# Kernel optimization log

Hardware: AMD Instinct MI355X
Metric: run time of the kernel (lower is better)

The kernel has to match this reference:

```python
import jax, jax.numpy as jnp
import numpy as np

J = 25
C_IN, HID, LAT = 3, 64, 32


def _graph_conv(x, A, W, b):
    # x: [N,T,J,Cin]; A: [J,J]; W: [Cin,Cout]; b: [Cout]
    A = jax.nn.softmax(A, axis=-1)
    # fused adjacency mix + projection: (A @ x) @ W + b
    x = jnp.einsum('ij,ntjc->ntic', A, x)
    return jnp.einsum('ntjc,cd->ntjd', x, W) + b


def setup_inputs() -> dict:
    key = jax.random.key(0)
    ks = jax.random.split(key, 13)
    x = jax.random.normal(ks[0], (32, 2048, J, C_IN), dtype=jnp.float32)
    eye = jnp.eye(J, dtype=jnp.float32)
    def lin(kw, kb, cin, cout):
        W = jax.random.normal(kw, (cin, cout), dtype=jnp.float32) / np.sqrt(cin)
        b = jax.random.normal(kb, (cout,), dtype=jnp.float32) * 0.01
        return W, b
    W1, b1 = lin(ks[1], ks[2], C_IN, HID)
    W2, b2 = lin(ks[3], ks[4], HID, LAT)
    W3, b3 = lin(ks[5], ks[6], LAT, HID)
    W4, b4 = lin(ks[7], ks[8], HID, C_IN)
    return {
        'x': x,
        'A1': eye, 'W1': W1, 'b1': b1,
        'A2': eye, 'W2': W2, 'b2': b2,
        'A3': eye, 'W3': W3, 'b3': b3,
        'A4': eye, 'W4': W4, 'b4': b4,
    }


def reference(x, A1, W1, b1, A2, W2, b2, A3, W3, b3, A4, W4, b4):
    h = jax.nn.relu(_graph_conv(x, A1, W1, b1))     # encoder_g1 + relu
    z = _graph_conv(h, A2, W2, b2)                  # encoder_g2 (no relu)
    h_dec = jax.nn.relu(_graph_conv(z, A3, W3, b3)) # decoder_g1 + relu
    out = _graph_conv(h_dec, A4, W4, b4)            # decoder_g2
    return out
```

## Files before the change

### kernel.cpp

```cpp
#include <hip/hip_runtime.h>
#include <math.h>

#define J 25
#define NJC 75
#define NWAVE 4
#define NTHREADS 256
#define NFPW 8
#define SCRW 1056

#define O_A1T  0
#define O_APP  1024
#define O_A4B  2048
#define O_W2T  3072
#define O_W3T  5120
#define O_W1T  7168
#define O_W4C  8192
#define O_BPPB 8448
#define O_B4   8512

using bf16x4 = __attribute__((ext_vector_type(4))) __bf16;
using bf16x8 = __attribute__((ext_vector_type(8))) __bf16;
using f32x16 = __attribute__((ext_vector_type(16))) float;

__device__ inline bf16x8 zero8() {
    bf16x8 z;
    #pragma unroll
    for (int j = 0; j < 8; j++) z[j] = (__bf16)0.f;
    return z;
}

__device__ inline unsigned pkbf(float a, float b) {
    union { __bf16 h; unsigned short u; } ua, ub;
    ua.h = (__bf16)a; ub.h = (__bf16)b;
    return (unsigned)ua.u | ((unsigned)ub.u << 16);
}

__device__ inline void cswap(const f32x16 acc, int half, int lx,
                             bf16x8* f0, bf16x8* f1) {
    const unsigned p0 = pkbf(acc[0],  acc[1]),  p1 = pkbf(acc[2],  acc[3]);
    const unsigned p2 = pkbf(acc[4],  acc[5]),  p3 = pkbf(acc[6],  acc[7]);
    const unsigned p4 = pkbf(acc[8],  acc[9]),  p5 = pkbf(acc[10], acc[11]);
    const unsigned p6 = pkbf(acc[12], acc[13]), p7 = pkbf(acc[14], acc[15]);
    const unsigned s0 = half ? p0 : p2, s1 = half ? p1 : p3;
    const unsigned s2 = half ? p4 : p6, s3 = half ? p5 : p7;
    const unsigned r0 = (unsigned)__shfl((int)s0, lx, 64);
    const unsigned r1 = (unsigned)__shfl((int)s1, lx, 64);
    const unsigned r2 = (unsigned)__shfl((int)s2, lx, 64);
    const unsigned r3 = (unsigned)__shfl((int)s3, lx, 64);
    uint4 u0, u1;
    u0.x = half ? r0 : p0;  u0.y = half ? r1 : p1;
    u0.z = half ? p2 : r0;  u0.w = half ? p3 : r1;
    u1.x = half ? r2 : p4;  u1.y = half ? r3 : p5;
    u1.z = half ? p6 : r2;  u1.w = half ? p7 : r3;
    *f0 = *(bf16x8*)&u0;  *f1 = *(bf16x8*)&u1;
}

__global__ void gcn_precompute(
    const float* __restrict__ A1, const float* __restrict__ W1, const float* __restrict__ b1,
    const float* __restrict__ A2, const float* __restrict__ W2, const float* __restrict__ b2,
    const float* __restrict__ A3, const float* __restrict__ W3, const float* __restrict__ b3,
    const float* __restrict__ A4, const float* __restrict__ W4, const float* __restrict__ b4,
    __bf16* __restrict__ cw)
{
    __shared__ float T[3125];
    __shared__ float bpp[64];
    float* T0 = T;        float* T1 = T + 625;  float* T2 = T + 1250;
    float* T3 = T + 1875; float* T4 = T + 2500;
    const int t = threadIdx.x;

    if (t < 100) {
        const int m = t / J, i = t % J;
        const float* Asrc = (m == 0) ? A1 : (m == 1) ? A2 : (m == 2) ? A3 : A4;
        float row[J];
        float mx = -1e30f;
        #pragma unroll
        for (int j = 0; j < J; j++) { row[j] = Asrc[i * J + j]; mx = fmaxf(mx, row[j]); }
        float s = 0.f;
        #pragma unroll
        for (int j = 0; j < J; j++) { row[j] = __expf(row[j] - mx); s += row[j]; }
        const float inv = 1.f / s;
        float* dst = T + m * 625 + i * J;
        #pragma unroll
        for (int j = 0; j < J; j++) dst[j] = row[j] * inv;
    }
    if (t < 64) {
        float s = b3[t];
        #pragma unroll
        for (int l = 0; l < 32; l++) s += W3[l * 64 + t] * b2[l];
        bpp[t] = s;
    }
    __syncthreads();

    for (int idx = t; idx < 625; idx += 256) {
        const int i = idx / J, jj = idx % J;
        float s = 0.f;
        #pragma unroll
        for (int k = 0; k < J; k++) s += T2[i * J + k] * T1[k * J + jj];
        T4[idx] = s;
    }
    __syncthreads();

    for (int i = t; i < 1024; i += 256) {
        const int b = i >> 8, n = (i >> 3) & 31, jj = i & 7, j = 8 * b + jj;
        const bool ok = (j < J) && (n < J);
        cw[O_A1T + i] = (__bf16)(ok ? T0[n * J + j] : 0.f);
        cw[O_APP + i] = (__bf16)(ok ? T4[n * J + j] : 0.f);
        cw[O_A4B + i] = (__bf16)(ok ? T3[n * J + j] : 0.f);
    }
    for (int i = t; i < 2048; i += 256) {
        const int b = i >> 8, m = (i >> 3) & 31, jj = i & 7;
        cw[O_W2T + i] = (__bf16)W2[(8 * b + jj) * 32 + m];
        const int tt = i >> 10, r = i & 1023;
        const int b3i = r >> 8, m3 = (r >> 3) & 31, j3 = r & 7;
        cw[O_W3T + i] = (__bf16)W3[(8 * b3i + j3) * 64 + tt * 32 + m3];
    }
    for (int i = t; i < 1024; i += 256) {
        const int tt = i >> 9, r = i & 511, hf = r >> 8, q = r & 255;
        const int m = q >> 3, c = q & 7, d = tt * 32 + m;
        float v = 0.f;
        if (hf == 0) {
            if (c < 3) v = W1[c * 64 + d];
            else if (c == 3) v = b1[d];
        }
        cw[O_W1T + i] = (__bf16)v;
    }
    if (t < 256)
        cw[O_W4C + t] = (t < 192) ? (__bf16)W4[(t & 63) * 3 + (t >> 6)] : (__bf16)0.f;

    if (t < 64) {
        const int tt = t >> 5, rem = t & 31, hf = rem >> 4, q = rem & 15;
        const int g = q >> 2, r2 = q & 3;
        cw[O_BPPB + t] = (__bf16)bpp[tt * 32 + 8 * g + 4 * hf + r2];
    }
    float* fb4 = (float*)(cw + O_B4);
    if (t >= 64 && t < 68) fb4[t - 64] = (t < 67) ? b4[t - 64] : 0.f;
}

__global__ __launch_bounds__(NTHREADS, 3) void gcn_fused(
    const float* __restrict__ x,
    const __bf16* __restrict__ cw,
    float* __restrict__ out)
{
    __shared__ __align__(16) __bf16 SCR[NWAVE * SCRW];

    const int t = threadIdx.x;
    const int w = t >> 6, lane = t & 63, ln = lane & 31, half = lane >> 5;
    const int lx = lane ^ 32;
    const int fo = ln * 8;
    __bf16* sc = &SCR[w * SCRW];

    const long fbase = ((long)blockIdx.x * NWAVE + w) * NFPW;

    long xb = fbase * NJC;
    float xv0 = x[xb + lane];
    float xv1 = (lane < NJC - 64) ? x[xb + 64 + lane] : 0.f;

    bf16x8 rA1T[2], rApp[2], rA4b[2], rW1[2], rW2[4], rW3[4], rW4[4], rBpp[4];
    #pragma unroll
    for (int ks = 0; ks < 2; ks++) {
        rA1T[ks] = *(const bf16x8*)&cw[O_A1T + (2 * ks + half) * 256 + fo];
        rApp[ks] = *(const bf16x8*)&cw[O_APP + (2 * ks + half) * 256 + fo];
        rA4b[ks] = *(const bf16x8*)&cw[O_A4B + (2 * ks + half) * 256 + fo];
        rW1[ks]  = *(const bf16x8*)&cw[O_W1T + ks * 512 + half * 256 + fo];
    }
    #pragma unroll
    for (int ks = 0; ks < 4; ks++)
        rW2[ks] = *(const bf16x8*)&cw[O_W2T + (half + 2 * ks) * 256 + fo];
    #pragma unroll
    for (int tt = 0; tt < 2; tt++)
        #pragma unroll
        for (int ks = 0; ks < 2; ks++)
            rW3[tt * 2 + ks] = *(const bf16x8*)&cw[O_W3T + tt * 1024 + (half + 2 * ks) * 256 + fo];
    #pragma unroll
    for (int ks = 0; ks < 4; ks++) {
        rW4[ks] = zero8();
        if (ln < 3) rW4[ks] = *(const bf16x8*)&cw[O_W4C + ln * 64 + (half + 2 * ks) * 8];
    }
    #pragma unroll
    for (int tt = 0; tt < 2; tt++)
        #pragma unroll
        for (int p = 0; p < 2; p++)
            rBpp[tt * 2 + p] = *(const bf16x8*)&cw[O_BPPB + (tt * 2 + half) * 16 + p * 8];
    float b4v = 0.f;
    if (ln < 3) b4v = ((const float*)(cw + O_B4))[ln];

    f32x16 Z;
    #pragma unroll
    for (int z = 0; z < 16; z++) Z[z] = 0.f;

    for (int fi = 0; fi < NFPW; fi++) {
        const long f = fbase + fi;

        {
            const int i0 = lane, c0 = i0 % 3, j0 = i0 / 3;
            sc[(j0 >> 3) * 264 + c0 * 8 + (j0 & 7)] = (__bf16)xv0;
            if (lane < NJC - 64) {
                const int i1 = 64 + lane, c1 = i1 % 3, j1 = i1 / 3;
                sc[(j1 >> 3) * 264 + c1 * 8 + (j1 & 7)] = (__bf16)xv1;
            }
            if (half == 0) sc[(ln >> 3) * 264 + 24 + (ln & 7)] = (ln < J) ? (__bf16)1.f : (__bf16)0.f;
            if (lane < 21) sc[3 * 264 + (lane / 7) * 8 + 1 + (lane % 7)] = (__bf16)0.f;
        }

        float nxv0 = 0.f, nxv1 = 0.f;
        if (fi + 1 < NFPW) {
            const long nxb = (f + 1) * NJC;
            nxv0 = x[nxb + lane];
            if (lane < NJC - 64) nxv1 = x[nxb + 64 + lane];
        }

        f32x16 accY;
        {
            bf16x8 a0 = *(const bf16x8*)&sc[half * 264 + fo];
            accY = __builtin_amdgcn_mfma_f32_32x32x16_bf16(a0, rA1T[0], Z, 0, 0, 0);
            bf16x8 a1 = *(const bf16x8*)&sc[(2 + half) * 264 + fo];
            accY = __builtin_amdgcn_mfma_f32_32x32x16_bf16(a1, rA1T[1], accY, 0, 0, 0);
        }

        bf16x8 yb;
        #pragma unroll
        for (int jj = 0; jj < 8; jj++)
            yb[jj] = (half == 0 && jj < 4) ? (__bf16)accY[jj] : (__bf16)0.f;
        bf16x8 hf[4];
        #pragma unroll
        for (int tt = 0; tt < 2; tt++) {
            f32x16 acc = __builtin_amdgcn_mfma_f32_32x32x16_bf16(rW1[tt], yb, Z, 0, 0, 0);
            #pragma unroll
            for (int z = 0; z < 16; z++) acc[z] = fmaxf(acc[z], 0.f);
            cswap(acc, half, lx, &hf[tt * 2], &hf[tt * 2 + 1]);
        }

        f32x16 accU = __builtin_amdgcn_mfma_f32_32x32x16_bf16(hf[0], rW2[0], Z, 0, 0, 0);
        #pragma unroll
        for (int ks = 1; ks < 4; ks++)
            accU = __builtin_amdgcn_mfma_f32_32x32x16_bf16(hf[ks], rW2[ks], accU, 0, 0, 0);
        bf16x8 uf[2];
        cswap(accU, half, lx, &uf[0], &uf[1]);

        f32x16 accV = __builtin_amdgcn_mfma_f32_32x32x16_bf16(uf[0], rApp[0], Z, 0, 0, 0);
        accV = __builtin_amdgcn_mfma_f32_32x32x16_bf16(uf[1], rApp[1], accV, 0, 0, 0);
        bf16x8 vf[2];
        cswap(accV, half, lx, &vf[0], &vf[1]);

        bf16x8 hd[4];
        #pragma unroll
        for (int tt = 0; tt < 2; tt++) {
            f32x16 acc = __builtin_amdgcn_mfma_f32_32x32x16_bf16(rW3[tt * 2 + 0], vf[0], Z, 0, 0, 0);
            acc = __builtin_amdgcn_mfma_f32_32x32x16_bf16(rW3[tt * 2 + 1], vf[1], acc, 0, 0, 0);
            #pragma unroll
            for (int q = 0; q < 16; q++) {
                const float bias = (float)rBpp[tt * 2 + (q >> 3)][q & 7];
                acc[q] = fmaxf(acc[q] + bias, 0.f);
            }
            cswap(acc, half, lx, &hd[tt * 2], &hd[tt * 2 + 1]);
        }

        f32x16 accP = __builtin_amdgcn_mfma_f32_32x32x16_bf16(hd[0], rW4[0], Z, 0, 0, 0);
        #pragma unroll
        for (int ks = 1; ks < 4; ks++)
            accP = __builtin_amdgcn_mfma_f32_32x32x16_bf16(hd[ks], rW4[ks], accP, 0, 0, 0);
        bf16x8 pf[2];
        cswap(accP, half, lx, &pf[0], &pf[1]);

        f32x16 accO = __builtin_amdgcn_mfma_f32_32x32x16_bf16(rA4b[0], pf[0], Z, 0, 0, 0);
        accO = __builtin_amdgcn_mfma_f32_32x32x16_bf16(rA4b[1], pf[1], accO, 0, 0, 0);
        if (ln < 3) {
            const long ob = f * NJC;
            #pragma unroll
            for (int r = 0; r < 16; r++) {
                const int row = (r & 3) + 8 * (r >> 2) + 4 * half;
                if (row < J) out[ob + row * 3 + ln] = accO[r] + b4v;
            }
        }

        xv0 = nxv0; xv1 = nxv1;
    }
}

extern "C" void kernel_launch(void* const* d_in, const int* in_sizes, int n_in,
                              void* d_out, int out_size, void* d_ws, size_t ws_size,
                              hipStream_t stream)
{
    const float* x  = (const float*)d_in[0];
    const float* A1 = (const float*)d_in[1];
    const float* W1 = (const float*)d_in[2];
    const float* b1 = (const float*)d_in[3];
    const float* A2 = (const float*)d_in[4];
    const float* W2 = (const float*)d_in[5];
    const float* b2 = (const float*)d_in[6];
    const float* A3 = (const float*)d_in[7];
    const float* W3 = (const float*)d_in[8];
    const float* b3 = (const float*)d_in[9];
    const float* A4 = (const float*)d_in[10];
    const float* W4 = (const float*)d_in[11];
    const float* b4 = (const float*)d_in[12];
    float* out = (float*)d_out;
    __bf16* cw = (__bf16*)d_ws;

    const int NT = in_sizes[0] / NJC;
    const int nblocks = NT / (NWAVE * NFPW);

    gcn_precompute<<<1, 256, 0, stream>>>(
        A1, W1, b1, A2, W2, b2, A3, W3, b3, A4, W4, b4, cw);
    gcn_fused<<<nblocks, NTHREADS, 0, stream>>>(x, cw, out);
}
```

Baseline: 165.5 us.

## Permute precomputed weight layouts to drop cross-lane shuffles between MFMA stages

Reorders the K dimension of the precomputed adjacency and weight matrices to match the MFMA accumulator row layout. Each stage's f32 accumulator can then be packed straight into bf16 operands for the next MFMA, with no __shfl-based half swap. The constant padding writes into the scratch tile are hoisted out of the frame loop. Frames per wave drop from 8 to 4, so the grid doubles, and the launch bound's min-blocks hint goes from 3 to 2, which may change register allocation and occupancy.

```diff
diff --git a/kernel.cpp b/kernel.cpp
--- a/kernel.cpp
+++ b/kernel.cpp
@@ -5,7 +5,7 @@
 #define NJC 75
 #define NWAVE 4
 #define NTHREADS 256
-#define NFPW 8
+#define NFPW 4
 #define SCRW 1056
 
 #define O_A1T  0
@@ -18,7 +18,6 @@
 #define O_BPPB 8448
 #define O_B4   8512
 
-using bf16x4 = __attribute__((ext_vector_type(4))) __bf16;
 using bf16x8 = __attribute__((ext_vector_type(8))) __bf16;
 using f32x16 = __attribute__((ext_vector_type(16))) float;
 
@@ -29,31 +28,6 @@
     return z;
 }
 
-__device__ inline unsigned pkbf(float a, float b) {
-    union { __bf16 h; unsigned short u; } ua, ub;
-    ua.h = (__bf16)a; ub.h = (__bf16)b;
-    return (unsigned)ua.u | ((unsigned)ub.u << 16);
-}
-
-__device__ inline void cswap(const f32x16 acc, int half, int lx,
-                             bf16x8* f0, bf16x8* f1) {
-    const unsigned p0 = pkbf(acc[0],  acc[1]),  p1 = pkbf(acc[2],  acc[3]);
-    const unsigned p2 = pkbf(acc[4],  acc[5]),  p3 = pkbf(acc[6],  acc[7]);
-    const unsigned p4 = pkbf(acc[8],  acc[9]),  p5 = pkbf(acc[10], acc[11]);
-    const unsigned p6 = pkbf(acc[12], acc[13]), p7 = pkbf(acc[14], acc[15]);
-    const unsigned s0 = half ? p0 : p2, s1 = half ? p1 : p3;
-    const unsigned s2 = half ? p4 : p6, s3 = half ? p5 : p7;
-    const unsigned r0 = (unsigned)__shfl((int)s0, lx, 64);
-    const unsigned r1 = (unsigned)__shfl((int)s1, lx, 64);
-    const unsigned r2 = (unsigned)__shfl((int)s2, lx, 64);
-    const unsigned r3 = (unsigned)__shfl((int)s3, lx, 64);
-    uint4 u0, u1;
-    u0.x = half ? r0 : p0;  u0.y = half ? r1 : p1;
-    u0.z = half ? p2 : r0;  u0.w = half ? p3 : r1;
-    u1.x = half ? r2 : p4;  u1.y = half ? r3 : p5;
-    u1.z = half ? p6 : r2;  u1.w = half ? p7 : r3;
-    *f0 = *(bf16x8*)&u0;  *f1 = *(bf16x8*)&u1;
-}
 
 __global__ void gcn_precompute(
     const float* __restrict__ A1, const float* __restrict__ W1, const float* __restrict__ b1,
@@ -101,18 +75,28 @@
     __syncthreads();
 
     for (int i = t; i < 1024; i += 256) {
-        const int b = i >> 8, n = (i >> 3) & 31, jj = i & 7, j = 8 * b + jj;
-        const bool ok = (j < J) && (n < J);
-        cw[O_A1T + i] = (__bf16)(ok ? T0[n * J + j] : 0.f);
-        cw[O_APP + i] = (__bf16)(ok ? T4[n * J + j] : 0.f);
-        cw[O_A4B + i] = (__bf16)(ok ? T3[n * J + j] : 0.f);
+        const int b = i >> 8, n = (i >> 3) & 31, jj = i & 7;
+        const int kn = 8 * b + jj;
+        cw[O_A1T + i] = (__bf16)((kn < J && n < J) ? T0[n * J + kn] : 0.f);
+        const int s = b >> 1, h = b & 1, r = 8 * s + jj;
+        const int k32 = (r & 3) + 8 * (r >> 2) + 4 * h;
+        cw[O_APP + i] = (__bf16)((k32 < J && n < J) ? T4[n * J + k32] : 0.f);
+        cw[O_A4B + i] = (__bf16)((k32 < J && n < J) ? T3[n * J + k32] : 0.f);
     }
     for (int i = t; i < 2048; i += 256) {
-        const int b = i >> 8, m = (i >> 3) & 31, jj = i & 7;
-        cw[O_W2T + i] = (__bf16)W2[(8 * b + jj) * 32 + m];
-        const int tt = i >> 10, r = i & 1023;
-        const int b3i = r >> 8, m3 = (r >> 3) & 31, j3 = r & 7;
-        cw[O_W3T + i] = (__bf16)W3[(8 * b3i + j3) * 64 + tt * 32 + m3];
+        {
+            const int b = i >> 8, n = (i >> 3) & 31, jj = i & 7;
+            const int s = b >> 1, h = b & 1, r = 8 * (s & 1) + jj;
+            const int d = 32 * (s >> 1) + (r & 3) + 8 * (r >> 2) + 4 * h;
+            cw[O_W2T + i] = (__bf16)W2[d * 32 + n];
+        }
+        {
+            const int tt = i >> 10, rr = i & 1023;
+            const int b = rr >> 8, m = (rr >> 3) & 31, jj = rr & 7;
+            const int s = b >> 1, h = b & 1, r = 8 * s + jj;
+            const int l = (r & 3) + 8 * (r >> 2) + 4 * h;
+            cw[O_W3T + i] = (__bf16)W3[l * 64 + tt * 32 + m];
+        }
     }
     for (int i = t; i < 1024; i += 256) {
         const int tt = i >> 9, r = i & 511, hf = r >> 8, q = r & 255;
@@ -124,19 +108,21 @@
         }
         cw[O_W1T + i] = (__bf16)v;
     }
-    if (t < 256)
-        cw[O_W4C + t] = (t < 192) ? (__bf16)W4[(t & 63) * 3 + (t >> 6)] : (__bf16)0.f;
-
+    if (t < 256) {
+        const int c = t >> 6, b = (t >> 3) & 7, jj = t & 7;
+        const int s = b >> 1, h = b & 1, r = 8 * (s & 1) + jj;
+        const int d = 32 * (s >> 1) + (r & 3) + 8 * (r >> 2) + 4 * h;
+        cw[O_W4C + t] = (c < 3) ? (__bf16)W4[d * 3 + c] : (__bf16)0.f;
+    }
     if (t < 64) {
         const int tt = t >> 5, rem = t & 31, hf = rem >> 4, q = rem & 15;
-        const int g = q >> 2, r2 = q & 3;
-        cw[O_BPPB + t] = (__bf16)bpp[tt * 32 + 8 * g + 4 * hf + r2];
+        cw[O_BPPB + t] = (__bf16)bpp[tt * 32 + (q & 3) + 8 * (q >> 2) + 4 * hf];
     }
     float* fb4 = (float*)(cw + O_B4);
     if (t >= 64 && t < 68) fb4[t - 64] = (t < 67) ? b4[t - 64] : 0.f;
 }
 
-__global__ __launch_bounds__(NTHREADS, 3) void gcn_fused(
+__global__ __launch_bounds__(NTHREADS, 2) void gcn_fused(
     const float* __restrict__ x,
     const __bf16* __restrict__ cw,
     float* __restrict__ out)
@@ -145,7 +131,6 @@
 
     const int t = threadIdx.x;
     const int w = t >> 6, lane = t & 63, ln = lane & 31, half = lane >> 5;
-    const int lx = lane ^ 32;
     const int fo = ln * 8;
     __bf16* sc = &SCR[w * SCRW];
 
@@ -154,6 +139,9 @@
     long xb = fbase * NJC;
     float xv0 = x[xb + lane];
     float xv1 = (lane < NJC - 64) ? x[xb + 64 + lane] : 0.f;
+
+    if (half == 0) sc[(ln >> 3) * 264 + 24 + (ln & 7)] = (ln < J) ? (__bf16)1.f : (__bf16)0.f;
+    if (lane < 21) sc[3 * 264 + (lane / 7) * 8 + 1 + (lane % 7)] = (__bf16)0.f;
 
     bf16x8 rA1T[2], rApp[2], rA4b[2], rW1[2], rW2[4], rW3[4], rW4[4], rBpp[4];
     #pragma unroll
@@ -188,19 +176,16 @@
     #pragma unroll
     for (int z = 0; z < 16; z++) Z[z] = 0.f;
 
+    const int c0 = lane % 3, j0 = lane / 3;
+    const int sc0 = (j0 >> 3) * 264 + c0 * 8 + (j0 & 7);
+    const int i1 = 64 + lane, c1 = i1 % 3, j1 = i1 / 3;
+    const int sc1 = (j1 >> 3) * 264 + c1 * 8 + (j1 & 7);
+
     for (int fi = 0; fi < NFPW; fi++) {
         const long f = fbase + fi;
 
-        {
-            const int i0 = lane, c0 = i0 % 3, j0 = i0 / 3;
-            sc[(j0 >> 3) * 264 + c0 * 8 + (j0 & 7)] = (__bf16)xv0;
-            if (lane < NJC - 64) {
-                const int i1 = 64 + lane, c1 = i1 % 3, j1 = i1 / 3;
-                sc[(j1 >> 3) * 264 + c1 * 8 + (j1 & 7)] = (__bf16)xv1;
-            }
-            if (half == 0) sc[(ln >> 3) * 264 + 24 + (ln & 7)] = (ln < J) ? (__bf16)1.f : (__bf16)0.f;
-            if (lane < 21) sc[3 * 264 + (lane / 7) * 8 + 1 + (lane % 7)] = (__bf16)0.f;
-        }
+        sc[sc0] = (__bf16)xv0;
+        if (lane < NJC - 64) sc[sc1] = (__bf16)xv1;
 
         float nxv0 = 0.f, nxv1 = 0.f;
         if (fi + 1 < NFPW) {
@@ -209,13 +194,10 @@
             if (lane < NJC - 64) nxv1 = x[nxb + 64 + lane];
         }
 
-        f32x16 accY;
-        {
-            bf16x8 a0 = *(const bf16x8*)&sc[half * 264 + fo];
-            accY = __builtin_amdgcn_mfma_f32_32x32x16_bf16(a0, rA1T[0], Z, 0, 0, 0);
-            bf16x8 a1 = *(const bf16x8*)&sc[(2 + half) * 264 + fo];
-            accY = __builtin_amdgcn_mfma_f32_32x32x16_bf16(a1, rA1T[1], accY, 0, 0, 0);
-        }
+        bf16x8 a0 = *(const bf16x8*)&sc[half * 264 + fo];
+        bf16x8 a1 = *(const bf16x8*)&sc[(2 + half) * 264 + fo];
+        f32x16 accY = __builtin_amdgcn_mfma_f32_32x32x16_bf16(a0, rA1T[0], Z, 0, 0, 0);
+        accY = __builtin_amdgcn_mfma_f32_32x32x16_bf16(a1, rA1T[1], accY, 0, 0, 0);
 
         bf16x8 yb;
         #pragma unroll
@@ -226,21 +208,29 @@
         for (int tt = 0; tt < 2; tt++) {
             f32x16 acc = __builtin_amdgcn_mfma_f32_32x32x16_bf16(rW1[tt], yb, Z, 0, 0, 0);
             #pragma unroll
-            for (int z = 0; z < 16; z++) acc[z] = fmaxf(acc[z], 0.f);
-            cswap(acc, half, lx, &hf[tt * 2], &hf[tt * 2 + 1]);
+            for (int st = 0; st < 2; st++)
+                #pragma unroll
+                for (int jj = 0; jj < 8; jj++)
+                    hf[2 * tt + st][jj] = (__bf16)fmaxf(acc[8 * st + jj], 0.f);
         }
 
         f32x16 accU = __builtin_amdgcn_mfma_f32_32x32x16_bf16(hf[0], rW2[0], Z, 0, 0, 0);
         #pragma unroll
-        for (int ks = 1; ks < 4; ks++)
-            accU = __builtin_amdgcn_mfma_f32_32x32x16_bf16(hf[ks], rW2[ks], accU, 0, 0, 0);
+        for (int s = 1; s < 4; s++)
+            accU = __builtin_amdgcn_mfma_f32_32x32x16_bf16(hf[s], rW2[s], accU, 0, 0, 0);
         bf16x8 uf[2];
-        cswap(accU, half, lx, &uf[0], &uf[1]);
+        #pragma unroll
+        for (int s = 0; s < 2; s++)
+            #pragma unroll
+            for (int jj = 0; jj < 8; jj++) uf[s][jj] = (__bf16)accU[8 * s + jj];
 
         f32x16 accV = __builtin_amdgcn_mfma_f32_32x32x16_bf16(uf[0], rApp[0], Z, 0, 0, 0);
         accV = __builtin_amdgcn_mfma_f32_32x32x16_bf16(uf[1], rApp[1], accV, 0, 0, 0);
         bf16x8 vf[2];
-        cswap(accV, half, lx, &vf[0], &vf[1]);
+        #pragma unroll
+        for (int s = 0; s < 2; s++)
+            #pragma unroll
+            for (int jj = 0; jj < 8; jj++) vf[s][jj] = (__bf16)accV[8 * s + jj];
 
         bf16x8 hd[4];
         #pragma unroll
@@ -248,19 +238,23 @@
             f32x16 acc = __builtin_amdgcn_mfma_f32_32x32x16_bf16(rW3[tt * 2 + 0], vf[0], Z, 0, 0, 0);
             acc = __builtin_amdgcn_mfma_f32_32x32x16_bf16(rW3[tt * 2 + 1], vf[1], acc, 0, 0, 0);
             #pragma unroll
-            for (int q = 0; q < 16; q++) {
-                const float bias = (float)rBpp[tt * 2 + (q >> 3)][q & 7];
-                acc[q] = fmaxf(acc[q] + bias, 0.f);
-            }
-            cswap(acc, half, lx, &hd[tt * 2], &hd[tt * 2 + 1]);
+            for (int st = 0; st < 2; st++)
+                #pragma unroll
+                for (int jj = 0; jj < 8; jj++) {
+                    const float bias = (float)rBpp[2 * tt + st][jj];
+                    hd[2 * tt + st][jj] = (__bf16)fmaxf(acc[8 * st + jj] + bias, 0.f);
+                }
         }
 
         f32x16 accP = __builtin_amdgcn_mfma_f32_32x32x16_bf16(hd[0], rW4[0], Z, 0, 0, 0);
         #pragma unroll
-        for (int ks = 1; ks < 4; ks++)
-            accP = __builtin_amdgcn_mfma_f32_32x32x16_bf16(hd[ks], rW4[ks], accP, 0, 0, 0);
+        for (int s = 1; s < 4; s++)
+            accP = __builtin_amdgcn_mfma_f32_32x32x16_bf16(hd[s], rW4[s], accP, 0, 0, 0);
         bf16x8 pf[2];
-        cswap(accP, half, lx, &pf[0], &pf[1]);
+        #pragma unroll
+        for (int s = 0; s < 2; s++)
+            #pragma unroll
+            for (int jj = 0; jj < 8; jj++) pf[s][jj] = (__bf16)accP[8 * s + jj];
 
         f32x16 accO = __builtin_amdgcn_mfma_f32_32x32x16_bf16(rA4b[0], pf[0], Z, 0, 0, 0);
         accO = __builtin_amdgcn_mfma_f32_32x32x16_bf16(rA4b[1], pf[1], accO, 0, 0, 0);
```

Result: faster. 146.8 us (-11.3%).
